# Optimization experiments

Measured on AMD Instinct MI355X. Metric: run time of the kernel, lower is better.

Reference implementation:

```python
import jax, jax.numpy as jnp
import numpy as np

K = 16  # number of neighbors (self excluded), matches init k
NUM_CLASSES = 100


def setup_inputs() -> dict:
    key = jax.random.key(0)
    kx, ky = jax.random.split(key)
    N, D = 8192, 256
    x = jax.random.normal(kx, (N, D), dtype=jnp.float32)
    y = jax.random.randint(ky, (N,), 0, NUM_CLASSES, dtype=jnp.int64)
    return {"x": x, "y": y}


def _knn_loss(x, y):
    N = x.shape[0]
    k = min(K, N - 1)
    # Pairwise squared Euclidean distances via Gram trick: [N, N]
    sq_norms = jnp.sum(x * x, axis=1)
    sq = sq_norms[:, None] + sq_norms[None, :] - 2.0 * (x @ x.T)
    sq = jnp.maximum(sq, 0.0)
    eye = jnp.eye(N, dtype=bool)
    # Keep sqrt grad-safe on the (excluded) diagonal by placing a dummy 1.0 there.
    d = jnp.sqrt(jnp.where(eye, 1.0, sq))  # [N, N] Euclidean distances

    # k nearest neighbors excluding self (BallTree query k+1 then drop col 0).
    d_for_knn = jnp.where(eye, jnp.inf, d)
    _, nn_idx = jax.lax.top_k(-d_for_knn, k)  # [N, k] indices of smallest distances

    # distances = exp(-d); denominator sums over all j != i.
    exp_d = jnp.where(eye, 0.0, jnp.exp(-d))
    denom = jnp.sum(exp_d, axis=1)  # [N]

    # log(exp(-d_in) / denom_i) = -d_in - log(denom_i)
    nn_d = jnp.take_along_axis(d, nn_idx, axis=1)          # [N, k]
    log_p = -nn_d - jnp.log(denom)[:, None]                 # [N, k]

    # Only neighbors with matching label contribute; rows with none are skipped.
    match = (y[nn_idx] == y[:, None]).astype(x.dtype)       # [N, k]
    cnt = jnp.sum(match, axis=1)                            # [N]
    row_mean = jnp.where(cnt > 0, jnp.sum(log_p * match, axis=1) / jnp.maximum(cnt, 1.0), 0.0)
    return -jnp.sum(row_mean) / N


def reference(x, y):
    return _knn_loss(x, y)
```

## Files before the change

### kernel.cpp

```cpp
#include <hip/hip_runtime.h>
#include <hip/hip_fp16.h>


typedef __attribute__((ext_vector_type(8))) short s8v;
typedef __attribute__((ext_vector_type(4))) float f32x4;
typedef __attribute__((ext_vector_type(2))) unsigned u32x2;
typedef __attribute__((ext_vector_type(4))) unsigned u32x4;

#define NROW 8192
#define NK   256

template <bool B> struct BoolC { static constexpr bool value = B; };

#define OFF_DNP  0
#define OFF_NRM  262144
#define OFF_XB   294912
#define OFF_CAND (294912 + 4194304)

__device__ __forceinline__ unsigned short f2bf(float f) {
  unsigned u = __float_as_uint(f);
  return (unsigned short)((u + 0x7FFFu + ((u >> 16) & 1u)) >> 16);
}

__device__ __forceinline__ void gld16(const void* g, void* l) {
  __builtin_amdgcn_global_load_lds(
      (const __attribute__((address_space(1))) unsigned int*)g,
      (__attribute__((address_space(3))) unsigned int*)l, 16, 0, 0);
}

__device__ __forceinline__ unsigned umin32(unsigned a, unsigned b) { return a < b ? a : b; }
__device__ __forceinline__ unsigned umax32(unsigned a, unsigned b) { return a > b ? a : b; }

__global__ __launch_bounds__(256) void k_prep(const float* __restrict__ x,
                                              unsigned short* __restrict__ xb,
                                              float* __restrict__ nrm) {
  const int w = threadIdx.x >> 6, l = threadIdx.x & 63;
  const int r = blockIdx.x * 4 + w;
  const float4 xv = *reinterpret_cast<const float4*>(x + r * NK + l * 4);
  float ns = xv.x * xv.x + xv.y * xv.y + xv.z * xv.z + xv.w * xv.w;
  ns += __shfl_xor(ns, 1);  ns += __shfl_xor(ns, 2);  ns += __shfl_xor(ns, 4);
  ns += __shfl_xor(ns, 8);  ns += __shfl_xor(ns, 16); ns += __shfl_xor(ns, 32);
  if (l == 0) nrm[r] = ns;
  ushort4 bv;
  bv.x = f2bf(xv.x); bv.y = f2bf(xv.y); bv.z = f2bf(xv.z); bv.w = f2bf(xv.w);
  const int gs = (l >> 1) ^ (r & 7);
  *reinterpret_cast<ushort4*>(xb + r * NK + gs * 8 + (l & 1) * 4) = bv;
}

__global__ __launch_bounds__(256, 4) void k_main(const unsigned short* __restrict__ xb,
                                                 const float* __restrict__ nrm,
                                                 float* __restrict__ dnp,
                                                 unsigned* __restrict__ cand) {
  __shared__ __align__(16) unsigned short Bl[64 * NK];
  __shared__ float ncsAll[1024];
  __shared__ float dpart[64];
  const int tid = threadIdx.x;
  const int w = tid >> 6, l = tid & 63, l15 = l & 15, l4 = l >> 4;
  const int rb = blockIdx.x >> 3, cs = blockIdx.x & 7;
  const int rowbase = rb * 64 + (w >> 1) * 32;
  const int wcol = (w & 1) * 32;
  const int colslice = cs * 1024;

  if (tid < 64) dpart[tid] = 0.0f;
  #pragma unroll
  for (int j = 0; j < 4; ++j)
    ncsAll[tid + j * 256] = nrm[colslice + tid + j * 256];

  s8v A[2][8];
  #pragma unroll
  for (int rf = 0; rf < 2; ++rf) {
    const int rr = rowbase + rf * 16 + l15;
    #pragma unroll
    for (int kf = 0; kf < 8; ++kf) {
      const int g = ((kf << 2) | l4) ^ (rr & 7);
      A[rf][kf] = *reinterpret_cast<const s8v*>(xb + rr * NK + g * 8);
    }
  }
  float nr[2][4], dn[2][4];
  unsigned s0[2][4], s1[2][4];
  #pragma unroll
  for (int rf = 0; rf < 2; ++rf)
    #pragma unroll
    for (int q = 0; q < 4; ++q) {
      nr[rf][q] = nrm[rowbase + rf * 16 + l4 * 4 + q];
      dn[rf][q] = 0.0f;
      s0[rf][q] = 0xFFFFFFFFu;
      s1[rf][q] = 0xFFFFFFFFu;
    }

  auto stage = [&](int t) {
    const unsigned short* src = xb + (colslice + t * 64) * NK;
    #pragma unroll
    for (int jj = 0; jj < 8; ++jj)
      gld16(src + (jj * 256 + tid) * 8, &Bl[(jj * 256 + w * 64) * 8]);
  };

  const int dtb = rowbase - colslice;
  const int tdw = (dtb >= 0 && dtb < 1024) ? (dtb >> 6) : -1;

  for (int t = 0; t < 16; ++t) {
    stage(t);
    __syncthreads();
    const int cbase = colslice + t * 64;
    f32x4 acc[2][2];
    #pragma unroll
    for (int rf = 0; rf < 2; ++rf) {
      f32x4 z = {0.f, 0.f, 0.f, 0.f};
      acc[rf][0] = z; acc[rf][1] = z;
    }
    #pragma unroll
    for (int kf = 0; kf < 8; ++kf) {
      const int gs = ((kf << 2) | l4) ^ (l15 & 7);
      const s8v b0 = *reinterpret_cast<const s8v*>(&Bl[(wcol + l15) * NK + gs * 8]);
      const s8v b1 = *reinterpret_cast<const s8v*>(&Bl[(wcol + 16 + l15) * NK + gs * 8]);
      #pragma unroll
      for (int rf = 0; rf < 2; ++rf) {
        acc[rf][0] = __builtin_amdgcn_mfma_f32_16x16x32_bf16(A[rf][kf], b0, acc[rf][0], 0, 0, 0);
        acc[rf][1] = __builtin_amdgcn_mfma_f32_16x16x32_bf16(A[rf][kf], b1, acc[rf][1], 0, 0, 0);
      }
    }
    const float nc0 = ncsAll[t * 64 + wcol + l15];
    const float nc1 = ncsAll[t * 64 + wcol + 16 + l15];
    const unsigned colg0 = (unsigned)(cbase + wcol + l15);
    const unsigned colg1 = colg0 + 16;
    auto epi = [&](auto dgc) {
      constexpr bool DG = decltype(dgc)::value;
      #pragma unroll
      for (int rf = 0; rf < 2; ++rf)
        #pragma unroll
        for (int q = 0; q < 4; ++q) {
          const unsigned rowg = (unsigned)(rowbase + rf * 16 + l4 * 4 + q);
          float sq0 = fmaf(acc[rf][0][q], -2.0f, nr[rf][q] + nc0);
          float sq1 = fmaf(acc[rf][1][q], -2.0f, nr[rf][q] + nc1);
          if (DG) { sq0 = fmaxf(sq0, 0.0f); sq1 = fmaxf(sq1, 0.0f); }
          const float d0 = __builtin_amdgcn_sqrtf(sq0);
          const float d1 = __builtin_amdgcn_sqrtf(sq1);
          float e0 = __expf(-d0), e1 = __expf(-d1);
          unsigned k0 = ((unsigned)__half_as_ushort(__float2half(d0)) << 16) | colg0;
          unsigned k1 = ((unsigned)__half_as_ushort(__float2half(d1)) << 16) | colg1;
          if (DG) {
            const bool nd0 = (rowg != colg0), nd1 = (rowg != colg1);
            e0 = nd0 ? e0 : 0.0f;          e1 = nd1 ? e1 : 0.0f;
            k0 = nd0 ? k0 : 0xFFFFFFFFu;   k1 = nd1 ? k1 : 0xFFFFFFFFu;
          }
          dn[rf][q] += e0 + e1;
          unsigned ev = umax32(s0[rf][q], k0);
          s0[rf][q] = umin32(s0[rf][q], k0);
          s1[rf][q] = umin32(s1[rf][q], ev);
          ev = umax32(s0[rf][q], k1);
          s0[rf][q] = umin32(s0[rf][q], k1);
          s1[rf][q] = umin32(s1[rf][q], ev);
        }
    };
    if (t == tdw) epi(BoolC<true>{});
    else          epi(BoolC<false>{});
    __syncthreads();
  }
  #pragma unroll
  for (int rf = 0; rf < 2; ++rf)
    #pragma unroll
    for (int q = 0; q < 4; ++q) {
      const int rowg = rowbase + rf * 16 + l4 * 4 + q;
      u32x2 pr; pr.x = s0[rf][q]; pr.y = s1[rf][q];
      __builtin_nontemporal_store(pr,
          reinterpret_cast<u32x2*>(&cand[rowg * 512 + cs * 64 + (w & 1) * 32 + l15 * 2]));
    }
  #pragma unroll
  for (int rf = 0; rf < 2; ++rf)
    #pragma unroll
    for (int q = 0; q < 4; ++q) {
      float vs = dn[rf][q];
      vs += __shfl_xor(vs, 1); vs += __shfl_xor(vs, 2);
      vs += __shfl_xor(vs, 4); vs += __shfl_xor(vs, 8);
      if (l15 == 0) atomicAdd(&dpart[(w >> 1) * 32 + rf * 16 + l4 * 4 + q], vs);
    }
  __syncthreads();
  if (tid < 64) dnp[(rb * 64 + tid) * 8 + cs] = dpart[tid];
}

__global__ __launch_bounds__(256) void k_fin(const unsigned* __restrict__ cand,
                                             const float* __restrict__ dnp,
                                             const int* __restrict__ y,
                                             float* __restrict__ out) {
  const int w = threadIdx.x >> 6, l = threadIdx.x & 63;
  const int r = blockIdx.x * 4 + w;
  unsigned kk[8];
  const u32x4 pa = __builtin_nontemporal_load(
      reinterpret_cast<const u32x4*>(cand + r * 512 + l * 8));
  const u32x4 pb = __builtin_nontemporal_load(
      reinterpret_cast<const u32x4*>(cand + r * 512 + l * 8 + 4));
  kk[0] = pa.x; kk[1] = pa.y; kk[2] = pa.z; kk[3] = pa.w;
  kk[4] = pb.x; kk[5] = pb.y; kk[6] = pb.z; kk[7] = pb.w;
  unsigned myKey = 0xFFFFFFFFu;
  for (int pp = 0; pp < 16; ++pp) {
    unsigned lm = kk[0];
    #pragma unroll
    for (int j = 1; j < 8; ++j) lm = umin32(lm, kk[j]);
    unsigned m = lm;
    m = umin32(m, __shfl_xor(m, 1));  m = umin32(m, __shfl_xor(m, 2));
    m = umin32(m, __shfl_xor(m, 4));  m = umin32(m, __shfl_xor(m, 8));
    m = umin32(m, __shfl_xor(m, 16)); m = umin32(m, __shfl_xor(m, 32));
    const unsigned long long bal = __ballot(lm == m);
    const int owner = (int)__ffsll(bal) - 1;
    if (l == owner) {
      bool f = false;
      #pragma unroll
      for (int j = 0; j < 8; ++j)
        if (!f && kk[j] == m) { kk[j] = 0xFFFFFFFFu; f = true; }
    }
    if (l == pp) myKey = m;
  }
  float den = 0.0f;
  #pragma unroll
  for (int cs = 0; cs < 8; ++cs) den += dnp[r * 8 + cs];
  const float logden = __logf(den);
  float contrib = 0.0f, cmf = 0.0f;
  if (l < 16 && myKey != 0xFFFFFFFFu) {
    const int col = (int)(myKey & 0x1FFFu);
    const float dd = __half2float(__ushort_as_half((unsigned short)(myKey >> 16)));
    if (y[col] == y[r]) { contrib = -dd - logden; cmf = 1.0f; }
  }
  contrib += __shfl_xor(contrib, 1);  contrib += __shfl_xor(contrib, 2);
  contrib += __shfl_xor(contrib, 4);  contrib += __shfl_xor(contrib, 8);
  contrib += __shfl_xor(contrib, 16); contrib += __shfl_xor(contrib, 32);
  cmf += __shfl_xor(cmf, 1);  cmf += __shfl_xor(cmf, 2);
  cmf += __shfl_xor(cmf, 4);  cmf += __shfl_xor(cmf, 8);
  cmf += __shfl_xor(cmf, 16); cmf += __shfl_xor(cmf, 32);
  if (l == 0 && cmf > 0.0f)
    atomicAdd(out, (contrib / cmf) * (-1.0f / 8192.0f));
}

extern "C" void kernel_launch(void* const* d_in, const int* in_sizes, int n_in,
                              void* d_out, int out_size, void* d_ws, size_t ws_size,
                              hipStream_t stream) {
  const float* x = (const float*)d_in[0];
  const int* y = (const int*)d_in[1];
  float* out = (float*)d_out;
  char* ws = (char*)d_ws;

  float*          dnp  = (float*)(ws + OFF_DNP);
  float*          nrm  = (float*)(ws + OFF_NRM);
  unsigned short* xb   = (unsigned short*)(ws + OFF_XB);
  unsigned*       cand = (unsigned*)(ws + OFF_CAND);

  hipMemsetAsync(d_out, 0, sizeof(float), stream);
  k_prep<<<2048, 256, 0, stream>>>(x, xb, nrm);
  k_main<<<1024, 256, 0, stream>>>(xb, nrm, dnp, cand);
  k_fin <<<2048, 256, 0, stream>>>(cand, dnp, y, out);
}
```

Baseline: 113.8 us.

## Double-buffer column tiles in k_main with staggered start and fewer barriers

Splits the LDS B tile into two 32-column buffers and prefetches the next tile with global_load_lds while the current one is computed. This cuts the loop to one s_barrier per iteration, with manual vmcnt waits. Each block also starts at a staggered tile offset to spread memory traffic, and the output memset is folded into k_prep. The risk is that each wave only waits on its own loads before reading tiles that other waves filled, which could race, and the per-tile MFMA work is halved, so loop overhead counts for more.

```diff
diff --git a/kernel.cpp b/kernel.cpp
--- a/kernel.cpp
+++ b/kernel.cpp
@@ -33,7 +33,9 @@
 
 __global__ __launch_bounds__(256) void k_prep(const float* __restrict__ x,
                                               unsigned short* __restrict__ xb,
-                                              float* __restrict__ nrm) {
+                                              float* __restrict__ nrm,
+                                              float* __restrict__ out) {
+  if (blockIdx.x == 0 && threadIdx.x == 0) out[0] = 0.0f;
   const int w = threadIdx.x >> 6, l = threadIdx.x & 63;
   const int r = blockIdx.x * 4 + w;
   const float4 xv = *reinterpret_cast<const float4*>(x + r * NK + l * 4);
@@ -51,14 +53,14 @@
                                                  const float* __restrict__ nrm,
                                                  float* __restrict__ dnp,
                                                  unsigned* __restrict__ cand) {
-  __shared__ __align__(16) unsigned short Bl[64 * NK];
+  __shared__ __align__(16) unsigned short Bl[2][32 * NK];
   __shared__ float ncsAll[1024];
   __shared__ float dpart[64];
   const int tid = threadIdx.x;
   const int w = tid >> 6, l = tid & 63, l15 = l & 15, l4 = l >> 4;
   const int rb = blockIdx.x >> 3, cs = blockIdx.x & 7;
   const int rowbase = rb * 64 + (w >> 1) * 32;
-  const int wcol = (w & 1) * 32;
+  const int wcol = (w & 1) * 16;
   const int colslice = cs * 1024;
 
   if (tid < 64) dpart[tid] = 0.0f;
@@ -88,41 +90,45 @@
       s1[rf][q] = 0xFFFFFFFFu;
     }
 
-  auto stage = [&](int t) {
-    const unsigned short* src = xb + (colslice + t * 64) * NK;
-    #pragma unroll
-    for (int jj = 0; jj < 8; ++jj)
-      gld16(src + (jj * 256 + tid) * 8, &Bl[(jj * 256 + w * 64) * 8]);
+  auto stage = [&](int buf, int t) {
+    const unsigned short* src = xb + (colslice + t * 32) * NK;
+    #pragma unroll
+    for (int jj = 0; jj < 4; ++jj)
+      gld16(src + (jj * 256 + tid) * 8, &Bl[buf][(jj * 256 + tid) * 8]);
   };
 
   const int dtb = rowbase - colslice;
-  const int tdw = (dtb >= 0 && dtb < 1024) ? (dtb >> 6) : -1;
-
-  for (int t = 0; t < 16; ++t) {
-    stage(t);
-    __syncthreads();
-    const int cbase = colslice + t * 64;
-    f32x4 acc[2][2];
-    #pragma unroll
-    for (int rf = 0; rf < 2; ++rf) {
+  const int tdw = (dtb >= 0 && dtb < 1024) ? (dtb >> 5) : -1;
+  const int t0 = (((rb >> 2) + (rb >> 5)) & 3) * 8;
+
+  stage(0, t0);
+  for (int i = 0; i < 32; ++i) {
+    const int t = (t0 + i) & 31;
+    const int cur = i & 1;
+    __builtin_amdgcn_s_barrier();
+    __builtin_amdgcn_sched_barrier(0);
+    if (i + 1 < 32) {
+      stage(cur ^ 1, (t0 + i + 1) & 31);
+      asm volatile("s_waitcnt vmcnt(4)" ::: "memory");
+    } else {
+      asm volatile("s_waitcnt vmcnt(0)" ::: "memory");
+    }
+    __builtin_amdgcn_sched_barrier(0);
+    const int cbase = colslice + t * 32;
+    f32x4 acc[2];
+    {
       f32x4 z = {0.f, 0.f, 0.f, 0.f};
-      acc[rf][0] = z; acc[rf][1] = z;
+      acc[0] = z; acc[1] = z;
     }
     #pragma unroll
     for (int kf = 0; kf < 8; ++kf) {
       const int gs = ((kf << 2) | l4) ^ (l15 & 7);
-      const s8v b0 = *reinterpret_cast<const s8v*>(&Bl[(wcol + l15) * NK + gs * 8]);
-      const s8v b1 = *reinterpret_cast<const s8v*>(&Bl[(wcol + 16 + l15) * NK + gs * 8]);
-      #pragma unroll
-      for (int rf = 0; rf < 2; ++rf) {
-        acc[rf][0] = __builtin_amdgcn_mfma_f32_16x16x32_bf16(A[rf][kf], b0, acc[rf][0], 0, 0, 0);
-        acc[rf][1] = __builtin_amdgcn_mfma_f32_16x16x32_bf16(A[rf][kf], b1, acc[rf][1], 0, 0, 0);
-      }
-    }
-    const float nc0 = ncsAll[t * 64 + wcol + l15];
-    const float nc1 = ncsAll[t * 64 + wcol + 16 + l15];
+      const s8v b0 = *reinterpret_cast<const s8v*>(&Bl[cur][(wcol + l15) * NK + gs * 8]);
+      acc[0] = __builtin_amdgcn_mfma_f32_16x16x32_bf16(A[0][kf], b0, acc[0], 0, 0, 0);
+      acc[1] = __builtin_amdgcn_mfma_f32_16x16x32_bf16(A[1][kf], b0, acc[1], 0, 0, 0);
+    }
+    const float nc0 = ncsAll[t * 32 + wcol + l15];
     const unsigned colg0 = (unsigned)(cbase + wcol + l15);
-    const unsigned colg1 = colg0 + 16;
     auto epi = [&](auto dgc) {
       constexpr bool DG = decltype(dgc)::value;
       #pragma unroll
@@ -130,31 +136,24 @@
         #pragma unroll
         for (int q = 0; q < 4; ++q) {
           const unsigned rowg = (unsigned)(rowbase + rf * 16 + l4 * 4 + q);
-          float sq0 = fmaf(acc[rf][0][q], -2.0f, nr[rf][q] + nc0);
-          float sq1 = fmaf(acc[rf][1][q], -2.0f, nr[rf][q] + nc1);
-          if (DG) { sq0 = fmaxf(sq0, 0.0f); sq1 = fmaxf(sq1, 0.0f); }
+          float sq0 = fmaf(acc[rf][q], -2.0f, nr[rf][q] + nc0);
+          if (DG) sq0 = fmaxf(sq0, 0.0f);
           const float d0 = __builtin_amdgcn_sqrtf(sq0);
-          const float d1 = __builtin_amdgcn_sqrtf(sq1);
-          float e0 = __expf(-d0), e1 = __expf(-d1);
+          float e0 = __expf(-d0);
           unsigned k0 = ((unsigned)__half_as_ushort(__float2half(d0)) << 16) | colg0;
-          unsigned k1 = ((unsigned)__half_as_ushort(__float2half(d1)) << 16) | colg1;
           if (DG) {
-            const bool nd0 = (rowg != colg0), nd1 = (rowg != colg1);
-            e0 = nd0 ? e0 : 0.0f;          e1 = nd1 ? e1 : 0.0f;
-            k0 = nd0 ? k0 : 0xFFFFFFFFu;   k1 = nd1 ? k1 : 0xFFFFFFFFu;
+            const bool nd0 = (rowg != colg0);
+            e0 = nd0 ? e0 : 0.0f;
+            k0 = nd0 ? k0 : 0xFFFFFFFFu;
           }
-          dn[rf][q] += e0 + e1;
-          unsigned ev = umax32(s0[rf][q], k0);
+          dn[rf][q] += e0;
+          const unsigned ev = umax32(s0[rf][q], k0);
           s0[rf][q] = umin32(s0[rf][q], k0);
-          s1[rf][q] = umin32(s1[rf][q], ev);
-          ev = umax32(s0[rf][q], k1);
-          s0[rf][q] = umin32(s0[rf][q], k1);
           s1[rf][q] = umin32(s1[rf][q], ev);
         }
     };
     if (t == tdw) epi(BoolC<true>{});
     else          epi(BoolC<false>{});
-    __syncthreads();
   }
   #pragma unroll
   for (int rf = 0; rf < 2; ++rf)
@@ -243,8 +242,7 @@
   unsigned short* xb   = (unsigned short*)(ws + OFF_XB);
   unsigned*       cand = (unsigned*)(ws + OFF_CAND);
 
-  hipMemsetAsync(d_out, 0, sizeof(float), stream);
-  k_prep<<<2048, 256, 0, stream>>>(x, xb, nrm);
+  k_prep<<<2048, 256, 0, stream>>>(x, xb, nrm, out);
   k_main<<<1024, 256, 0, stream>>>(xb, nrm, dnp, cand);
   k_fin <<<2048, 256, 0, stream>>>(cand, dnp, y, out);
 }
```

Measured after the change: 139.3 us. 1.22x slower.
